# Performance work log

Measured on AMD Instinct MI355X. Metric: run time of the kernel, lower is better.

Reference implementation:

```python
import jax, jax.numpy as jnp
import numpy as np

B, S, D_IN, UNITS = 8, 2048, 512, 512


def _glorot(key, fan_in, fan_out):
    limit = np.sqrt(6.0 / (fan_in + fan_out)).astype(np.float32)
    return jax.random.uniform(key, (fan_in, fan_out), jnp.float32, -limit, limit)


def setup_inputs() -> dict:
    key = jax.random.key(0)
    kq, kwq, kwv, kwk = jax.random.split(key, 4)
    return {
        "query": jax.random.normal(kq, (B, S, D_IN), jnp.float32),
        "Wq": _glorot(kwq, D_IN, UNITS),   # W_query conv1d k=1, no bias
        "Wv": _glorot(kwv, D_IN, UNITS),   # W_value conv1d k=1, no bias
        "Wk": _glorot(kwk, D_IN, UNITS),   # W_key   conv1d k=1, no bias
    }


def reference(query, Wq, Wv, Wk):
    # Pointwise causal Conv1D(kernel=1, no bias) with sigmoid activation == sigmoid(x @ W)
    q = jax.nn.sigmoid(jnp.einsum('bsd,du->bsu', query, Wq))   # W_query(query)
    k = jax.nn.sigmoid(jnp.einsum('bsd,du->bsu', query, Wv))   # W_value(key=query)
    v = jax.nn.sigmoid(jnp.einsum('bsd,du->bsu', query, Wk))   # W_key(value=query)

    d_in = query.shape[-1]  # scaling uses value's input feature dim, not units
    score = jnp.einsum('bqu,bku->bqk', q, k) / jnp.sqrt(jnp.float32(d_in))  # [B,S,S]

    # Mask: upper triangle INCLUDING diagonal is -inf (strictly-causal, no self)
    s = score.shape[1]
    masked = jnp.where(jnp.triu(jnp.ones((s, s), bool)), -jnp.inf, score)

    # Row 0 is fully masked -> replaced by zeros; rows 1: softmax over j < i
    rest = jax.nn.softmax(masked[:, 1:, :], axis=-1)
    attn = jnp.concatenate([jnp.zeros((score.shape[0], 1, s), score.dtype), rest], axis=1)

    return jnp.einsum('bqk,bku->bqu', attn, v)
```

## Files before the change

### kernel.cpp

```cpp
#include <hip/hip_runtime.h>
#include <stdint.h>


typedef __attribute__((ext_vector_type(4))) float f32x4;
typedef __attribute__((ext_vector_type(8))) short short8;
typedef __attribute__((ext_vector_type(4))) short short4b;

__device__ __forceinline__ short f2bf(float f) {
    union { float f; uint32_t u; } v; v.f = f;
    uint32_t r = (v.u + 0x7FFFu + ((v.u >> 16) & 1u)) >> 16;
    return (short)r;
}
__device__ __forceinline__ float bf2f(short s) {
    union { uint32_t u; float f; } v; v.u = ((uint32_t)(uint16_t)s) << 16; return v.f;
}
__device__ __forceinline__ float sigm(float x) { return 1.0f / (1.0f + __expf(-x)); }

__device__ __forceinline__ void gload_lds16(const void* g, void* l) {
    __builtin_amdgcn_global_load_lds(
        (const __attribute__((address_space(1))) void*)g,
        (__attribute__((address_space(3))) void*)l, 16, 0, 0);
}

__global__ __launch_bounds__(256) void convert_x(
    const float* __restrict__ X, short* __restrict__ Xb)
{
    size_t i = (size_t)blockIdx.x * 256 + threadIdx.x;
    const float4* src = reinterpret_cast<const float4*>(X) + i * 2;
    float4 a = src[0], b = src[1];
    short8 o;
    o[0] = f2bf(a.x); o[1] = f2bf(a.y); o[2] = f2bf(a.z); o[3] = f2bf(a.w);
    o[4] = f2bf(b.x); o[5] = f2bf(b.y); o[6] = f2bf(b.z); o[7] = f2bf(b.w);
    *reinterpret_cast<short8*>(Xb + i * 8) = o;
}

__global__ __launch_bounds__(256) void prep_weights(
    const float* __restrict__ Wq, const float* __restrict__ Wv, const float* __restrict__ Wk,
    short* __restrict__ Wt)
{
    __shared__ float T[64 * 68];
    int bid = blockIdx.x;
    int w = bid >> 6;
    int tile = bid & 63;
    int n0 = (tile & 7) * 64;
    int k0 = (tile >> 3) * 64;
    const float* W = (w == 0) ? Wq : (w == 1) ? Wv : Wk;
    int t = threadIdx.x;
    int tr = t >> 4, tc = t & 15;
    for (int rr = 0; rr < 4; ++rr) {
        int row = rr * 16 + tr;
        float4 v = *reinterpret_cast<const float4*>(&W[(size_t)(k0 + row) * 512 + n0 + tc * 4]);
        T[row * 68 + tc * 4 + 0] = v.x;
        T[row * 68 + tc * 4 + 1] = v.y;
        T[row * 68 + tc * 4 + 2] = v.z;
        T[row * 68 + tc * 4 + 3] = v.w;
    }
    __syncthreads();
    for (int wr = 0; wr < 4; ++wr) {
        int nl = wr * 16 + tr;
        short4b o;
        for (int i = 0; i < 4; ++i) o[i] = f2bf(T[(tc * 4 + i) * 68 + nl]);
        *reinterpret_cast<short4b*>(&Wt[((size_t)(w * 512 + n0 + nl)) * 512 + k0 + tc * 4]) = o;
    }
}

__global__ __launch_bounds__(256) void qkv_gemm(
    const short* __restrict__ Xb,
    const short* __restrict__ Wt,
    short* __restrict__ Qb, short* __restrict__ Kb, short* __restrict__ VtG)
{
    __shared__ short SMEM[128 * 128];
    short* As = SMEM;
    short* Bs = SMEM + 128 * 64;

    int bx = blockIdx.x;
    int mt = bx & 127;
    int y = bx >> 7;
    int w = y >> 2, nt = y & 3;
    int m0 = mt * 128, n0 = nt * 128;

    int tid = threadIdx.x;
    int wv = tid >> 6, lane = tid & 63;
    int wr = wv >> 1, wc = wv & 1;
    int ln = lane & 15, hi = lane >> 4;

    f32x4 acc[4][4];
#pragma unroll
    for (int i = 0; i < 4; ++i)
#pragma unroll
        for (int j = 0; j < 4; ++j) acc[i][j] = {0.f, 0.f, 0.f, 0.f};

    const short* Asrc = Xb + (size_t)m0 * 512;
    const short* Bsrc = Wt + (size_t)w * 512 * 512 + (size_t)n0 * 512;

    for (int ko = 0; ko < 8; ++ko) {
        int k0 = ko * 64;
#pragma unroll
        for (int j = 0; j < 4; ++j) {
            int r = wv * 8 + j * 32 + (lane >> 3);
            int sc = ((lane & 7) * 8) ^ ((r & 7) << 3);
            gload_lds16(Asrc + (size_t)r * 512 + k0 + sc, &As[(wv * 8 + j * 32) * 64]);
        }
#pragma unroll
        for (int j = 0; j < 4; ++j) {
            int r = wv * 8 + j * 32 + (lane >> 3);
            int sc = ((lane & 7) * 8) ^ ((r & 7) << 3);
            gload_lds16(Bsrc + (size_t)r * 512 + k0 + sc, &Bs[(wv * 8 + j * 32) * 64]);
        }
        __syncthreads();
#pragma unroll
        for (int kk = 0; kk < 2; ++kk) {
            int kof = kk * 32 + hi * 8;
            int sw = (ln & 7) << 3;
            short8 af[4], bf[4];
#pragma unroll
            for (int mf = 0; mf < 4; ++mf)
                af[mf] = *reinterpret_cast<const short8*>(&As[(wr * 64 + mf * 16 + ln) * 64 + (kof ^ sw)]);
#pragma unroll
            for (int nf = 0; nf < 4; ++nf)
                bf[nf] = *reinterpret_cast<const short8*>(&Bs[(wc * 64 + nf * 16 + ln) * 64 + (kof ^ sw)]);
#pragma unroll
            for (int mf = 0; mf < 4; ++mf)
#pragma unroll
                for (int nf = 0; nf < 4; ++nf)
                    acc[mf][nf] = __builtin_amdgcn_mfma_f32_16x16x32_bf16(af[mf], bf[nf], acc[mf][nf], 0, 0, 0);
        }
        __syncthreads();
    }

    if (w < 2) {
        short* O = (w == 0) ? Qb : Kb;
#pragma unroll
        for (int mf = 0; mf < 4; ++mf)
#pragma unroll
            for (int nf = 0; nf < 4; ++nf)
#pragma unroll
                for (int j = 0; j < 4; ++j) {
                    int row = m0 + wr * 64 + mf * 16 + hi * 4 + j;
                    int col = n0 + wc * 64 + nf * 16 + ln;
                    O[(size_t)row * 512 + col] = f2bf(sigm(acc[mf][nf][j]));
                }
    } else {
#pragma unroll
        for (int mf = 0; mf < 4; ++mf)
#pragma unroll
            for (int nf = 0; nf < 4; ++nf)
#pragma unroll
                for (int j = 0; j < 4; ++j) {
                    int ml = wr * 64 + mf * 16 + hi * 4 + j;
                    int nl = wc * 64 + nf * 16 + ln;
                    SMEM[nl * 128 + (ml ^ ((nl & 7) << 3))] = f2bf(sigm(acc[mf][nf][j]));
                }
        __syncthreads();
        int bb = m0 >> 11;
        int s0 = m0 & 2047;
        int d = tid >> 1, h = tid & 1;
#pragma unroll
        for (int i = 0; i < 8; ++i) {
            int s8 = h * 64 + i * 8;
            short8 v = *reinterpret_cast<const short8*>(&SMEM[d * 128 + (s8 ^ ((d & 7) << 3))]);
            *reinterpret_cast<short8*>(&VtG[((size_t)(bb * 512 + n0 + d)) * 2048 + s0 + s8]) = v;
        }
    }
}

__global__ __launch_bounds__(256) void score_pass(
    const short* __restrict__ Qb, const short* __restrict__ Kb,
    short* __restrict__ Pc, float* __restrict__ Dpart)
{
    __shared__ short SMEM[128 * 128];
    __shared__ float psum[2][128];
    short* As = SMEM;
    short* Bs = SMEM + 128 * 64;

    const float scale = 0.044194173824159216f;

    int bid = blockIdx.x;
    int b = bid & 7;
    int idx = bid >> 3;
    int ti = 0;
    while ((ti + 1) * (ti + 2) / 2 <= idx) ++ti;
    int tj = idx - ti * (ti + 1) / 2;
    int m0 = ti * 128, n0 = tj * 128;

    int tid = threadIdx.x;
    int w = tid >> 6, lane = tid & 63;
    int wr = w >> 1, wc = w & 1;
    int ln = lane & 15, hi = lane >> 4;

    const short* Qsrc = Qb + (size_t)b * 2048 * 512 + (size_t)m0 * 512;
    const short* Ksrc = Kb + (size_t)b * 2048 * 512 + (size_t)n0 * 512;

    f32x4 acc[4][4];
#pragma unroll
    for (int i = 0; i < 4; ++i)
#pragma unroll
        for (int j = 0; j < 4; ++j) acc[i][j] = {0.f, 0.f, 0.f, 0.f};

    for (int ko = 0; ko < 8; ++ko) {
        int k0 = ko * 64;
#pragma unroll
        for (int j = 0; j < 4; ++j) {
            int r = w * 8 + j * 32 + (lane >> 3);
            int sc = ((lane & 7) * 8) ^ ((r & 7) << 3);
            gload_lds16(Qsrc + (size_t)r * 512 + k0 + sc, &As[(w * 8 + j * 32) * 64]);
        }
#pragma unroll
        for (int j = 0; j < 4; ++j) {
            int r = w * 8 + j * 32 + (lane >> 3);
            int sc = ((lane & 7) * 8) ^ ((r & 7) << 3);
            gload_lds16(Ksrc + (size_t)r * 512 + k0 + sc, &Bs[(w * 8 + j * 32) * 64]);
        }
        __syncthreads();
#pragma unroll
        for (int kk = 0; kk < 2; ++kk) {
            int kof = kk * 32 + hi * 8;
            int sw = (ln & 7) << 3;
            short8 af[4], bf[4];
#pragma unroll
            for (int mf = 0; mf < 4; ++mf)
                af[mf] = *reinterpret_cast<const short8*>(&As[(wr * 64 + mf * 16 + ln) * 64 + (kof ^ sw)]);
#pragma unroll
            for (int nf = 0; nf < 4; ++nf)
                bf[nf] = *reinterpret_cast<const short8*>(&Bs[(wc * 64 + nf * 16 + ln) * 64 + (kof ^ sw)]);
#pragma unroll
            for (int mf = 0; mf < 4; ++mf)
#pragma unroll
                for (int nf = 0; nf < 4; ++nf)
                    acc[mf][nf] = __builtin_amdgcn_mfma_f32_16x16x32_bf16(af[mf], bf[nf], acc[mf][nf], 0, 0, 0);
        }
        __syncthreads();
    }

    short* Ptile = Pc + (size_t)(b * 136 + idx) * 128 * 128;
#pragma unroll
    for (int mf = 0; mf < 4; ++mf) {
        float rs[4] = {0.f, 0.f, 0.f, 0.f};
#pragma unroll
        for (int nf = 0; nf < 4; ++nf)
#pragma unroll
            for (int j = 0; j < 4; ++j) {
                int rl = wr * 64 + mf * 16 + hi * 4 + j;
                int cl = wc * 64 + nf * 16 + ln;
                int irow = m0 + rl, jcol = n0 + cl;
                float p = (jcol < irow) ? __expf(acc[mf][nf][j] * scale) : 0.f;
                short hs = f2bf(p);
                Ptile[(size_t)rl * 128 + cl] = hs;
                rs[j] += bf2f(hs);
            }
#pragma unroll
        for (int j = 0; j < 4; ++j) {
            float s = rs[j];
            s += __shfl_xor(s, 1);
            s += __shfl_xor(s, 2);
            s += __shfl_xor(s, 4);
            s += __shfl_xor(s, 8);
            if (ln == 0) psum[wc][wr * 64 + mf * 16 + hi * 4 + j] = s;
        }
    }
    __syncthreads();
    if (tid < 128)
        Dpart[((size_t)b * 16 + tj) * 2048 + m0 + tid] = psum[0][tid] + psum[1][tid];
}

__global__ __launch_bounds__(256) void pv_pass(
    const short* __restrict__ Pc, const short* __restrict__ VtG,
    const float* __restrict__ Dpart, float* __restrict__ Out)
{
    __shared__ short SMEM[128 * 64 + 64 * 64];
    __shared__ float dnm[128];
    short* As = SMEM;
    short* Bs = SMEM + 128 * 64;

    int bid = blockIdx.x;
    int b = bid & 7;
    int rr = bid >> 3;
    int grp = rr >> 5, off = rr & 31;
    int ti = (grp & 1) ? (15 - (off >> 1)) : (off >> 1);
    int colhalf = 2 * grp + (off & 1);
    int m0 = ti * 128, n0 = colhalf * 64;

    int tid = threadIdx.x;
    int w = tid >> 6, lane = tid & 63;
    int wr = w >> 1, wc = w & 1;
    int ln = lane & 15, hi = lane >> 4;

    if (tid < 128) {
        float s = 0.f;
        for (int tj = 0; tj <= ti; ++tj)
            s += Dpart[((size_t)b * 16 + tj) * 2048 + m0 + tid];
        int gi = m0 + tid;
        dnm[tid] = (gi == 0) ? 0.f : 1.0f / s;
    }

    const short* Ptiles = Pc + (size_t)(b * 136 + ti * (ti + 1) / 2) * 128 * 128;
    const short* Vsrc = VtG + (size_t)b * 512 * 2048 + (size_t)n0 * 2048;

    f32x4 acc[4][2];
#pragma unroll
    for (int i = 0; i < 4; ++i)
#pragma unroll
        for (int j = 0; j < 2; ++j) acc[i][j] = {0.f, 0.f, 0.f, 0.f};

    for (int ks = 0; ks < 2 * (ti + 1); ++ks) {
        int tj = ks >> 1;
        int j0 = (ks & 1) * 64;
        const short* Pt = Ptiles + (size_t)tj * 128 * 128;
#pragma unroll
        for (int j = 0; j < 4; ++j) {
            int r = w * 8 + j * 32 + (lane >> 3);
            int sc = ((lane & 7) * 8) ^ ((r & 7) << 3);
            gload_lds16(Pt + (size_t)r * 128 + j0 + sc, &As[(w * 8 + j * 32) * 64]);
        }
#pragma unroll
        for (int j = 0; j < 2; ++j) {
            int r = w * 8 + j * 32 + (lane >> 3);
            int sc = ((lane & 7) * 8) ^ ((r & 7) << 3);
            gload_lds16(Vsrc + (size_t)r * 2048 + tj * 128 + j0 + sc, &Bs[(w * 8 + j * 32) * 64]);
        }
        __syncthreads();
#pragma unroll
        for (int kk = 0; kk < 2; ++kk) {
            int kof = kk * 32 + hi * 8;
            int sw = (ln & 7) << 3;
            short8 af[4], bf[2];
#pragma unroll
            for (int mf = 0; mf < 4; ++mf)
                af[mf] = *reinterpret_cast<const short8*>(&As[(wr * 64 + mf * 16 + ln) * 64 + (kof ^ sw)]);
#pragma unroll
            for (int nf = 0; nf < 2; ++nf)
                bf[nf] = *reinterpret_cast<const short8*>(&Bs[(wc * 32 + nf * 16 + ln) * 64 + (kof ^ sw)]);
#pragma unroll
            for (int mf = 0; mf < 4; ++mf)
#pragma unroll
                for (int nf = 0; nf < 2; ++nf)
                    acc[mf][nf] = __builtin_amdgcn_mfma_f32_16x16x32_bf16(af[mf], bf[nf], acc[mf][nf], 0, 0, 0);
        }
        __syncthreads();
    }

#pragma unroll
    for (int mf = 0; mf < 4; ++mf)
#pragma unroll
        for (int j = 0; j < 4; ++j) {
            int rl = wr * 64 + mf * 16 + hi * 4 + j;
            float rd = dnm[rl];
            float* orow = Out + ((size_t)b * 2048 + m0 + rl) * 512 + n0 + wc * 32 + ln;
#pragma unroll
            for (int nf = 0; nf < 2; ++nf)
                orow[nf * 16] = acc[mf][nf][j] * rd;
        }
}

extern "C" void kernel_launch(void* const* d_in, const int* in_sizes, int n_in,
                              void* d_out, int out_size, void* d_ws, size_t ws_size,
                              hipStream_t stream) {
    const float* X  = (const float*)d_in[0];
    const float* Wq = (const float*)d_in[1];
    const float* Wv = (const float*)d_in[2];
    const float* Wk = (const float*)d_in[3];
    float* Out = (float*)d_out;

    char* ws = (char*)d_ws;
    const size_t WT_BYTES  = (size_t)3 * 512 * 512 * 2;
    const size_t MAT_BYTES = (size_t)16384 * 512 * 2;
    const size_t PC_BYTES  = (size_t)8 * 136 * 128 * 128 * 2;
    short* Wt = (short*)ws;
    short* Qb = (short*)(ws + WT_BYTES);
    short* Kb = (short*)(ws + WT_BYTES + MAT_BYTES);
    short* Vt = (short*)(ws + WT_BYTES + 2 * MAT_BYTES);
    short* Pc = (short*)(ws + WT_BYTES + 3 * MAT_BYTES);
    short* Xb = Pc;
    float* Dp = (float*)(ws + WT_BYTES + 3 * MAT_BYTES + PC_BYTES);

    convert_x<<<4096, 256, 0, stream>>>(X, Xb);
    prep_weights<<<192, 256, 0, stream>>>(Wq, Wv, Wk, Wt);
    qkv_gemm<<<1536, 256, 0, stream>>>(Xb, Wt, Qb, Kb, Vt);
    score_pass<<<1088, 256, 0, stream>>>(Qb, Kb, Pc, Dp);
    pv_pass<<<1024, 256, 0, stream>>>(Pc, Vt, Dp, Out);
}
```

Baseline: 137.1 us.

## Double-buffer LDS tiles in GEMM kernels and stage epilogue stores through LDS

All three GEMM-style kernels (QKV projection, score pass, PV pass) now use two LDS buffers. The next K-tile is issued via global_load_lds right after a combined vmcnt wait and barrier, which removes one barrier per iteration and overlaps loads with MFMA work. Epilogue writes of Q/K, P tiles and the fp32 output now go through swizzled LDS so global stores are 16-byte row-contiguous instead of scattered 2- or 4-byte stores. This doubles LDS use per block and adds a second launch_bounds occupancy hint. Occupancy may drop, and the single-barrier scheme depends on vmcnt covering the LDS-direct loads.

```diff
diff --git a/kernel.cpp b/kernel.cpp
--- a/kernel.cpp
+++ b/kernel.cpp
@@ -21,6 +21,8 @@
         (const __attribute__((address_space(1))) void*)g,
         (__attribute__((address_space(3))) void*)l, 16, 0, 0);
 }
+
+#define VMBAR() asm volatile("s_waitcnt vmcnt(0)\n\ts_barrier" ::: "memory")
 
 __global__ __launch_bounds__(256) void convert_x(
     const float* __restrict__ X, short* __restrict__ Xb)
@@ -64,14 +66,12 @@
     }
 }
 
-__global__ __launch_bounds__(256) void qkv_gemm(
+__global__ __launch_bounds__(256, 2) void qkv_gemm(
     const short* __restrict__ Xb,
     const short* __restrict__ Wt,
     short* __restrict__ Qb, short* __restrict__ Kb, short* __restrict__ VtG)
 {
-    __shared__ short SMEM[128 * 128];
-    short* As = SMEM;
-    short* Bs = SMEM + 128 * 64;
+    __shared__ short SMEM[2][16384];
 
     int bx = blockIdx.x;
     int mt = bx & 127;
@@ -93,21 +93,34 @@
     const short* Asrc = Xb + (size_t)m0 * 512;
     const short* Bsrc = Wt + (size_t)w * 512 * 512 + (size_t)n0 * 512;
 
+    int srow = wv * 8 + (lane >> 3);
+    int ssc0 = (lane & 7) * 8;
+
+#define QSTAGE(ko, buf)                                                            \
+    {                                                                              \
+        int _k0 = (ko) * 64;                                                       \
+        _Pragma("unroll")                                                          \
+        for (int _j = 0; _j < 4; ++_j) {                                           \
+            int _r = srow + _j * 32;                                               \
+            int _sc = ssc0 ^ ((_r & 7) << 3);                                      \
+            gload_lds16(Asrc + (size_t)_r * 512 + _k0 + _sc,                       \
+                        &SMEM[buf][(wv * 8 + _j * 32) * 64]);                      \
+        }                                                                          \
+        _Pragma("unroll")                                                          \
+        for (int _j = 0; _j < 4; ++_j) {                                           \
+            int _r = srow + _j * 32;                                               \
+            int _sc = ssc0 ^ ((_r & 7) << 3);                                      \
+            gload_lds16(Bsrc + (size_t)_r * 512 + _k0 + _sc,                       \
+                        &SMEM[buf][8192 + (wv * 8 + _j * 32) * 64]);               \
+        }                                                                          \
+    }
+
+    QSTAGE(0, 0);
     for (int ko = 0; ko < 8; ++ko) {
-        int k0 = ko * 64;
-#pragma unroll
-        for (int j = 0; j < 4; ++j) {
-            int r = wv * 8 + j * 32 + (lane >> 3);
-            int sc = ((lane & 7) * 8) ^ ((r & 7) << 3);
-            gload_lds16(Asrc + (size_t)r * 512 + k0 + sc, &As[(wv * 8 + j * 32) * 64]);
-        }
-#pragma unroll
-        for (int j = 0; j < 4; ++j) {
-            int r = wv * 8 + j * 32 + (lane >> 3);
-            int sc = ((lane & 7) * 8) ^ ((r & 7) << 3);
-            gload_lds16(Bsrc + (size_t)r * 512 + k0 + sc, &Bs[(wv * 8 + j * 32) * 64]);
-        }
-        __syncthreads();
+        VMBAR();
+        if (ko + 1 < 8) QSTAGE(ko + 1, (ko + 1) & 1);
+        const short* As = SMEM[ko & 1];
+        const short* Bs = SMEM[ko & 1] + 8192;
 #pragma unroll
         for (int kk = 0; kk < 2; ++kk) {
             int kof = kk * 32 + hi * 8;
@@ -125,21 +138,31 @@
                 for (int nf = 0; nf < 4; ++nf)
                     acc[mf][nf] = __builtin_amdgcn_mfma_f32_16x16x32_bf16(af[mf], bf[nf], acc[mf][nf], 0, 0, 0);
         }
+    }
+    __syncthreads();
+#undef QSTAGE
+
+    short* Ts = SMEM[0];
+    if (w < 2) {
+#pragma unroll
+        for (int mf = 0; mf < 4; ++mf)
+#pragma unroll
+            for (int nf = 0; nf < 4; ++nf)
+#pragma unroll
+                for (int j = 0; j < 4; ++j) {
+                    int rl = wr * 64 + mf * 16 + hi * 4 + j;
+                    int cl = wc * 64 + nf * 16 + ln;
+                    Ts[rl * 128 + (cl ^ ((rl & 7) << 3))] = f2bf(sigm(acc[mf][nf][j]));
+                }
         __syncthreads();
-    }
-
-    if (w < 2) {
         short* O = (w == 0) ? Qb : Kb;
-#pragma unroll
-        for (int mf = 0; mf < 4; ++mf)
-#pragma unroll
-            for (int nf = 0; nf < 4; ++nf)
-#pragma unroll
-                for (int j = 0; j < 4; ++j) {
-                    int row = m0 + wr * 64 + mf * 16 + hi * 4 + j;
-                    int col = n0 + wc * 64 + nf * 16 + ln;
-                    O[(size_t)row * 512 + col] = f2bf(sigm(acc[mf][nf][j]));
-                }
+        int r = tid >> 1, h = tid & 1;
+#pragma unroll
+        for (int i = 0; i < 8; ++i) {
+            int c8 = h * 64 + i * 8;
+            short8 v = *reinterpret_cast<const short8*>(&Ts[r * 128 + (c8 ^ ((r & 7) << 3))]);
+            *reinterpret_cast<short8*>(&O[(size_t)(m0 + r) * 512 + n0 + c8]) = v;
+        }
     } else {
 #pragma unroll
         for (int mf = 0; mf < 4; ++mf)
@@ -149,7 +172,7 @@
                 for (int j = 0; j < 4; ++j) {
                     int ml = wr * 64 + mf * 16 + hi * 4 + j;
                     int nl = wc * 64 + nf * 16 + ln;
-                    SMEM[nl * 128 + (ml ^ ((nl & 7) << 3))] = f2bf(sigm(acc[mf][nf][j]));
+                    Ts[nl * 128 + (ml ^ ((nl & 7) << 3))] = f2bf(sigm(acc[mf][nf][j]));
                 }
         __syncthreads();
         int bb = m0 >> 11;
@@ -158,20 +181,18 @@
 #pragma unroll
         for (int i = 0; i < 8; ++i) {
             int s8 = h * 64 + i * 8;
-            short8 v = *reinterpret_cast<const short8*>(&SMEM[d * 128 + (s8 ^ ((d & 7) << 3))]);
+            short8 v = *reinterpret_cast<const short8*>(&Ts[d * 128 + (s8 ^ ((d & 7) << 3))]);
             *reinterpret_cast<short8*>(&VtG[((size_t)(bb * 512 + n0 + d)) * 2048 + s0 + s8]) = v;
         }
     }
 }
 
-__global__ __launch_bounds__(256) void score_pass(
+__global__ __launch_bounds__(256, 2) void score_pass(
     const short* __restrict__ Qb, const short* __restrict__ Kb,
     short* __restrict__ Pc, float* __restrict__ Dpart)
 {
-    __shared__ short SMEM[128 * 128];
+    __shared__ short SMEM[2][16384];
     __shared__ float psum[2][128];
-    short* As = SMEM;
-    short* Bs = SMEM + 128 * 64;
 
     const float scale = 0.044194173824159216f;
 
@@ -197,21 +218,34 @@
 #pragma unroll
         for (int j = 0; j < 4; ++j) acc[i][j] = {0.f, 0.f, 0.f, 0.f};
 
+    int srow = w * 8 + (lane >> 3);
+    int ssc0 = (lane & 7) * 8;
+
+#define SSTAGE(ko, buf)                                                            \
+    {                                                                              \
+        int _k0 = (ko) * 64;                                                       \
+        _Pragma("unroll")                                                          \
+        for (int _j = 0; _j < 4; ++_j) {                                           \
+            int _r = srow + _j * 32;                                               \
+            int _sc = ssc0 ^ ((_r & 7) << 3);                                      \
+            gload_lds16(Qsrc + (size_t)_r * 512 + _k0 + _sc,                       \
+                        &SMEM[buf][(w * 8 + _j * 32) * 64]);                       \
+        }                                                                          \
+        _Pragma("unroll")                                                          \
+        for (int _j = 0; _j < 4; ++_j) {                                           \
+            int _r = srow + _j * 32;                                               \
+            int _sc = ssc0 ^ ((_r & 7) << 3);                                      \
+            gload_lds16(Ksrc + (size_t)_r * 512 + _k0 + _sc,                       \
+                        &SMEM[buf][8192 + (w * 8 + _j * 32) * 64]);                \
+        }                                                                          \
+    }
+
+    SSTAGE(0, 0);
     for (int ko = 0; ko < 8; ++ko) {
-        int k0 = ko * 64;
-#pragma unroll
-        for (int j = 0; j < 4; ++j) {
-            int r = w * 8 + j * 32 + (lane >> 3);
-            int sc = ((lane & 7) * 8) ^ ((r & 7) << 3);
-            gload_lds16(Qsrc + (size_t)r * 512 + k0 + sc, &As[(w * 8 + j * 32) * 64]);
-        }
-#pragma unroll
-        for (int j = 0; j < 4; ++j) {
-            int r = w * 8 + j * 32 + (lane >> 3);
-            int sc = ((lane & 7) * 8) ^ ((r & 7) << 3);
-            gload_lds16(Ksrc + (size_t)r * 512 + k0 + sc, &Bs[(w * 8 + j * 32) * 64]);
-        }
-        __syncthreads();
+        VMBAR();
+        if (ko + 1 < 8) SSTAGE(ko + 1, (ko + 1) & 1);
+        const short* As = SMEM[ko & 1];
+        const short* Bs = SMEM[ko & 1] + 8192;
 #pragma unroll
         for (int kk = 0; kk < 2; ++kk) {
             int kof = kk * 32 + hi * 8;
@@ -229,10 +263,11 @@
                 for (int nf = 0; nf < 4; ++nf)
                     acc[mf][nf] = __builtin_amdgcn_mfma_f32_16x16x32_bf16(af[mf], bf[nf], acc[mf][nf], 0, 0, 0);
         }
-        __syncthreads();
-    }
-
-    short* Ptile = Pc + (size_t)(b * 136 + idx) * 128 * 128;
+    }
+    __syncthreads();
+#undef SSTAGE
+
+    short* Ts = SMEM[0];
 #pragma unroll
     for (int mf = 0; mf < 4; ++mf) {
         float rs[4] = {0.f, 0.f, 0.f, 0.f};
@@ -245,7 +280,7 @@
                 int irow = m0 + rl, jcol = n0 + cl;
                 float p = (jcol < irow) ? __expf(acc[mf][nf][j] * scale) : 0.f;
                 short hs = f2bf(p);
-                Ptile[(size_t)rl * 128 + cl] = hs;
+                Ts[rl * 128 + (cl ^ ((rl & 7) << 3))] = hs;
                 rs[j] += bf2f(hs);
             }
 #pragma unroll
@@ -259,6 +294,16 @@
         }
     }
     __syncthreads();
+    short* Ptile = Pc + (size_t)(b * 136 + idx) * 128 * 128;
+    {
+        int r = tid >> 1, h = tid & 1;
+#pragma unroll
+        for (int i = 0; i < 8; ++i) {
+            int c8 = h * 64 + i * 8;
+            short8 v = *reinterpret_cast<const short8*>(&Ts[r * 128 + (c8 ^ ((r & 7) << 3))]);
+            *reinterpret_cast<short8*>(&Ptile[(size_t)r * 128 + c8]) = v;
+        }
+    }
     if (tid < 128)
         Dpart[((size_t)b * 16 + tj) * 2048 + m0 + tid] = psum[0][tid] + psum[1][tid];
 }
@@ -267,10 +312,8 @@
     const short* __restrict__ Pc, const short* __restrict__ VtG,
     const float* __restrict__ Dpart, float* __restrict__ Out)
 {
-    __shared__ short SMEM[128 * 64 + 64 * 64];
+    __shared__ short SMEM[2][12288];
     __shared__ float dnm[128];
-    short* As = SMEM;
-    short* Bs = SMEM + 128 * 64;
 
     int bid = blockIdx.x;
     int b = bid & 7;
@@ -302,23 +345,37 @@
 #pragma unroll
         for (int j = 0; j < 2; ++j) acc[i][j] = {0.f, 0.f, 0.f, 0.f};
 
-    for (int ks = 0; ks < 2 * (ti + 1); ++ks) {
-        int tj = ks >> 1;
-        int j0 = (ks & 1) * 64;
-        const short* Pt = Ptiles + (size_t)tj * 128 * 128;
-#pragma unroll
-        for (int j = 0; j < 4; ++j) {
-            int r = w * 8 + j * 32 + (lane >> 3);
-            int sc = ((lane & 7) * 8) ^ ((r & 7) << 3);
-            gload_lds16(Pt + (size_t)r * 128 + j0 + sc, &As[(w * 8 + j * 32) * 64]);
-        }
-#pragma unroll
-        for (int j = 0; j < 2; ++j) {
-            int r = w * 8 + j * 32 + (lane >> 3);
-            int sc = ((lane & 7) * 8) ^ ((r & 7) << 3);
-            gload_lds16(Vsrc + (size_t)r * 2048 + tj * 128 + j0 + sc, &Bs[(w * 8 + j * 32) * 64]);
-        }
-        __syncthreads();
+    int srow = w * 8 + (lane >> 3);
+    int ssc0 = (lane & 7) * 8;
+    int nks = 2 * (ti + 1);
+
+#define PSTAGE(ks, buf)                                                            \
+    {                                                                              \
+        int _tj = (ks) >> 1;                                                       \
+        int _j0 = ((ks) & 1) * 64;                                                 \
+        const short* _Pt = Ptiles + (size_t)_tj * 128 * 128;                       \
+        _Pragma("unroll")                                                          \
+        for (int _j = 0; _j < 4; ++_j) {                                           \
+            int _r = srow + _j * 32;                                               \
+            int _sc = ssc0 ^ ((_r & 7) << 3);                                      \
+            gload_lds16(_Pt + (size_t)_r * 128 + _j0 + _sc,                        \
+                        &SMEM[buf][(w * 8 + _j * 32) * 64]);                       \
+        }                                                                          \
+        _Pragma("unroll")                                                          \
+        for (int _j = 0; _j < 2; ++_j) {                                           \
+            int _r = srow + _j * 32;                                               \
+            int _sc = ssc0 ^ ((_r & 7) << 3);                                      \
+            gload_lds16(Vsrc + (size_t)_r * 2048 + _tj * 128 + _j0 + _sc,          \
+                        &SMEM[buf][8192 + (w * 8 + _j * 32) * 64]);                \
+        }                                                                          \
+    }
+
+    PSTAGE(0, 0);
+    for (int ks = 0; ks < nks; ++ks) {
+        VMBAR();
+        if (ks + 1 < nks) PSTAGE(ks + 1, (ks + 1) & 1);
+        const short* As = SMEM[ks & 1];
+        const short* Bs = SMEM[ks & 1] + 8192;
 #pragma unroll
         for (int kk = 0; kk < 2; ++kk) {
             int kof = kk * 32 + hi * 8;
@@ -336,20 +393,32 @@
                 for (int nf = 0; nf < 2; ++nf)
                     acc[mf][nf] = __builtin_amdgcn_mfma_f32_16x16x32_bf16(af[mf], bf[nf], acc[mf][nf], 0, 0, 0);
         }
-        __syncthreads();
-    }
-
+    }
+    __syncthreads();
+#undef PSTAGE
+
+    float* Tf = reinterpret_cast<float*>(SMEM);
 #pragma unroll
     for (int mf = 0; mf < 4; ++mf)
 #pragma unroll
-        for (int j = 0; j < 4; ++j) {
-            int rl = wr * 64 + mf * 16 + hi * 4 + j;
-            float rd = dnm[rl];
-            float* orow = Out + ((size_t)b * 2048 + m0 + rl) * 512 + n0 + wc * 32 + ln;
-#pragma unroll
-            for (int nf = 0; nf < 2; ++nf)
-                orow[nf * 16] = acc[mf][nf][j] * rd;
-        }
+        for (int nf = 0; nf < 2; ++nf)
+#pragma unroll
+            for (int j = 0; j < 4; ++j) {
+                int rl = wr * 64 + mf * 16 + hi * 4 + j;
+                int cl = wc * 32 + nf * 16 + ln;
+                Tf[rl * 64 + (cl ^ ((rl & 7) << 2))] = acc[mf][nf][j] * dnm[rl];
+            }
+    __syncthreads();
+    {
+        int r = tid >> 1, h = tid & 1;
+        float* orow = Out + ((size_t)b * 2048 + m0 + r) * 512 + n0;
+#pragma unroll
+        for (int i = 0; i < 8; ++i) {
+            int c4 = (h * 8 + i) * 4;
+            float4 v = *reinterpret_cast<const float4*>(&Tf[r * 64 + (c4 ^ ((r & 7) << 2))]);
+            *reinterpret_cast<float4*>(&orow[c4]) = v;
+        }
+    }
 }
 
 extern "C" void kernel_launch(void* const* d_in, const int* in_sizes, int n_in,
```

Result: slower. 140.5 us (+2.5%).
